# Optimization experiments

Measured on AMD Instinct MI355X. Metric: run time of the kernel, lower is better.

Reference implementation:

```python
import jax, jax.numpy as jnp
import numpy as np

N_TOKEN = 267735
CUTS = [0, 20000, 40000, 200000, 267735]
DIV = 4
D_MODEL = 1024
N_HEAD = 16
D_HEAD = 64
D_INNER = 4096
N_LAYER = 4
QLEN = 512
MLEN = 512
BSZ = 4
EPS = 1e-5


def _ln(x, g, b):
    mu = jnp.mean(x, axis=-1, keepdims=True)
    var = jnp.var(x, axis=-1, keepdims=True)
    return (x - mu) * jax.lax.rsqrt(var + EPS) * g + b


def _rel_shift(x):
    # x: [qlen, klen, bsz, n_head]
    q, k, b, n = x.shape
    x = jnp.pad(x, ((0, 0), (1, 0), (0, 0), (0, 0)))
    x = x.reshape(k + 1, q, b, n)[1:]
    return x.reshape(q, k, b, n)


def setup_inputs() -> dict:
    key = jax.random.key(0)
    ks = list(jax.random.split(key, 32))
    p = lambda i, shape: 0.02 * jax.random.normal(ks[i], shape, dtype=jnp.float32)
    inp = {}
    inp['input_ids'] = jax.random.randint(ks[0], (BSZ, QLEN), 0, N_TOKEN, dtype=jnp.int32)
    inp['mems'] = 0.05 * jax.random.normal(ks[1], (N_LAYER, MLEN, BSZ, D_MODEL), dtype=jnp.float32)
    # adaptive embedding: cluster tables + projections (div_val=4)
    for i in range(4):
        l, r = CUTS[i], CUTS[i + 1]
        d_i = D_MODEL // (DIV ** i)
        inp[f'emb{i}'] = p(2 + i, (r - l, d_i))
        inp[f'proj{i}'] = p(6 + i, (d_i, D_MODEL))
    H = N_HEAD * D_HEAD
    inp['qkv_W'] = p(10, (N_LAYER, D_MODEL, 3 * H))
    inp['r_W'] = p(11, (N_LAYER, D_MODEL, H))
    inp['o_W'] = p(12, (N_LAYER, H, D_MODEL))
    inp['r_w_bias'] = p(13, (N_LAYER, N_HEAD, D_HEAD))
    inp['r_r_bias'] = p(14, (N_LAYER, N_HEAD, D_HEAD))
    inp['ln1_g'] = jnp.ones((N_LAYER, D_MODEL), jnp.float32)
    inp['ln1_b'] = jnp.zeros((N_LAYER, D_MODEL), jnp.float32)
    inp['ff_w1'] = p(15, (N_LAYER, D_MODEL, D_INNER))
    inp['ff_b1'] = jnp.zeros((N_LAYER, D_INNER), jnp.float32)
    inp['ff_w2'] = p(16, (N_LAYER, D_INNER, D_MODEL))
    inp['ff_b2'] = jnp.zeros((N_LAYER, D_MODEL), jnp.float32)
    inp['ln2_g'] = jnp.ones((N_LAYER, D_MODEL), jnp.float32)
    inp['ln2_b'] = jnp.zeros((N_LAYER, D_MODEL), jnp.float32)
    return inp


def _forward(input_ids, mems, embs, projs, qkv_W, r_W, o_W, r_w_bias, r_r_bias,
             ln1_g, ln1_b, ff_w1, ff_b1, ff_w2, ff_b2, ln2_g, ln2_b):
    ids = input_ids.T  # [qlen, bsz]
    qlen, bsz = ids.shape
    mems = jax.lax.stop_gradient(mems)  # mems are detached in the original
    mlen = mems.shape[1]
    klen = qlen + mlen

    # --- adaptive embedding (masked gather + scatter-add, same math as boolean_mask/scatter_nd) ---
    flat = ids.reshape(-1)
    emb = jnp.zeros((flat.shape[0], D_MODEL), jnp.float32)
    for i in range(4):
        l, r = CUTS[i], CUTS[i + 1]
        mask = (flat >= l) & (flat < r)
        idx = jnp.clip(flat - l, 0, r - l - 1)
        e_i = jnp.einsum('id,de->ie', embs[i][idx], projs[i])
        emb = emb + jnp.where(mask[:, None], e_i, 0.0)
    word_emb = (emb * (D_MODEL ** 0.5)).reshape(qlen, bsz, D_MODEL)

    # --- sinusoidal relative positions, pos_seq = klen-1 .. 0 ---
    pos_seq = jnp.arange(klen - 1, -1, -1, dtype=jnp.float32)
    inv_freq = 1.0 / (10000.0 ** (jnp.arange(0, D_MODEL, 2, dtype=jnp.float32) / D_MODEL))
    sinusoid = jnp.einsum('i,j->ij', pos_seq, inv_freq)
    pos_emb = jnp.concatenate([jnp.sin(sinusoid), jnp.cos(sinusoid)], axis=-1)  # [klen, d_model]

    # causal mask over memory-extended keys: [qlen, klen]
    attn_mask = jnp.triu(jnp.ones((qlen, klen), jnp.float32), k=1 + mlen)
    mask4 = attn_mask[:, :, None, None]
    scale = 1.0 / (D_HEAD ** 0.5)

    h = word_emb
    for l in range(N_LAYER):
        cat = jnp.concatenate([mems[l], h], axis=0)  # [klen, bsz, d_model]
        w_heads = jnp.einsum('kbd,dh->kbh', cat, qkv_W[l])
        r_head_k = jnp.einsum('kd,dh->kh', pos_emb, r_W[l]).reshape(klen, N_HEAD, D_HEAD)
        q_h, k_h, v_h = jnp.split(w_heads, 3, axis=-1)
        q_h = q_h[-qlen:].reshape(qlen, bsz, N_HEAD, D_HEAD)
        k_h = k_h.reshape(klen, bsz, N_HEAD, D_HEAD)
        v_h = v_h.reshape(klen, bsz, N_HEAD, D_HEAD)
        AC = jnp.einsum('ibnd,jbnd->ijbn', q_h + r_w_bias[l], k_h)
        BD = _rel_shift(jnp.einsum('ibnd,jnd->ijbn', q_h + r_r_bias[l], r_head_k))
        score = (AC + BD) * scale
        score = score * (1.0 - mask4) - 1e30 * mask4
        prob = jax.nn.softmax(score, axis=1)
        attn_vec = jnp.einsum('ijbn,jbnd->ibnd', prob, v_h).reshape(qlen, bsz, N_HEAD * D_HEAD)
        attn_out = jnp.einsum('ibh,hd->ibd', attn_vec, o_W[l])
        h = _ln(h + attn_out, ln1_g[l], ln1_b[l])
        ff = jnp.einsum('ibf,fd->ibd', jax.nn.relu(jnp.einsum('ibd,df->ibf', h, ff_w1[l]) + ff_b1[l]), ff_w2[l]) + ff_b2[l]
        h = _ln(h + ff, ln2_g[l], ln2_b[l])

    return h.transpose(1, 0, 2)  # [bsz, qlen, d_model]


def reference(input_ids, mems, emb0, emb1, emb2, emb3, proj0, proj1, proj2, proj3,
              qkv_W, r_W, o_W, r_w_bias, r_r_bias, ln1_g, ln1_b,
              ff_w1, ff_b1, ff_w2, ff_b2, ln2_g, ln2_b):
    return _forward(input_ids, mems, (emb0, emb1, emb2, emb3), (proj0, proj1, proj2, proj3),
                    qkv_W, r_W, o_W, r_w_bias, r_r_bias, ln1_g, ln1_b,
                    ff_w1, ff_b1, ff_w2, ff_b2, ln2_g, ln2_b)
```

## Files before the change

kernel.cpp:

```cpp
#include <hip/hip_runtime.h>

typedef __attribute__((ext_vector_type(8))) short bf16x8;
typedef __attribute__((ext_vector_type(4))) float f32x4;

#define N_LAYER 4
#define QLEN 512
#define MLEN 512
#define KLEN 1024
#define BSZ 4
#define DM 1024
#define NH 16
#define DH 64
#define DINNER 4096
#define EK 1408
#define BDLD 1152

__device__ __forceinline__ unsigned short f2bf(float x) {
    unsigned u = __float_as_uint(x);
    u += 0x7fffu + ((u >> 16) & 1u);
    return (unsigned short)(u >> 16);
}
__device__ __forceinline__ float bf2f(unsigned short v) {
    return __uint_as_float(((unsigned)v) << 16);
}

__device__ __forceinline__ void gload16(const unsigned short* g, unsigned short* l) {
    __builtin_amdgcn_global_load_lds(
        (const __attribute__((address_space(1))) unsigned int*)g,
        (__attribute__((address_space(3))) unsigned int*)l, 16, 0, 0);
}

__device__ __forceinline__ bf16x8 lds_read8_sw(const unsigned short* base, int row, int cb) {
    return *(const bf16x8*)((const char*)base + row * 128 + (cb ^ ((row & 7) << 4)));
}

__global__ __launch_bounds__(256)
void transpose_all(const float* __restrict__ qkvWl, const float* __restrict__ rWl,
                   const float* __restrict__ oWl, const float* __restrict__ w1l,
                   const float* __restrict__ w2l,
                   unsigned short* __restrict__ qkvT, unsigned short* __restrict__ rT,
                   unsigned short* __restrict__ oT, unsigned short* __restrict__ w1T,
                   unsigned short* __restrict__ w2T) {
    __shared__ float tile[32][33];
    int id = blockIdx.x;
    const float* W; unsigned short* D; int K, N, bx, by;
    if (id < 3072)      { W = qkvWl; D = qkvT; K = 1024; N = 3072; bx = id % 96;  by = id / 96; }
    else if (id < 4096) { id -= 3072; W = rWl;  D = rT;  K = 1024; N = 1024; bx = id & 31; by = id >> 5; }
    else if (id < 5120) { id -= 4096; W = oWl;  D = oT;  K = 1024; N = 1024; bx = id & 31; by = id >> 5; }
    else if (id < 9216) { id -= 5120; W = w1l;  D = w1T; K = 1024; N = 4096; bx = id & 127; by = id >> 7; }
    else                { id -= 9216; W = w2l;  D = w2T; K = 4096; N = 1024; bx = id & 31; by = id >> 5; }
    const int tx = threadIdx.x & 31, ty = threadIdx.x >> 5;
#pragma unroll
    for (int i = 0; i < 4; ++i)
        tile[ty + i * 8][tx] = W[(size_t)(by * 32 + ty + i * 8) * N + bx * 32 + tx];
    __syncthreads();
#pragma unroll
    for (int i = 0; i < 4; ++i)
        D[(size_t)(bx * 32 + ty + i * 8) * K + by * 32 + tx] = f2bf(tile[tx][ty + i * 8]);
}

__global__ __launch_bounds__(256)
void transpose_pad(const float* __restrict__ W, unsigned short* __restrict__ dst,
                   int K, int N, int dstLD, int dstOff) {
    __shared__ float tile[32][33];
    const int tx = threadIdx.x & 31, ty = threadIdx.x >> 5;
    const int bx = blockIdx.x, by = blockIdx.y;
#pragma unroll
    for (int i = 0; i < 4; ++i) {
        int k = by * 32 + ty + i * 8;
        tile[ty + i * 8][tx] = (k < K) ? W[(size_t)k * N + bx * 32 + tx] : 0.f;
    }
    __syncthreads();
#pragma unroll
    for (int i = 0; i < 4; ++i) {
        int n = bx * 32 + ty + i * 8;
        int k = by * 32 + tx;
        dst[(size_t)n * dstLD + dstOff + k] = f2bf(tile[tx][ty + i * 8]);
    }
}

__global__ __launch_bounds__(256)
void emb_gather(const int* __restrict__ ids,
                const float* __restrict__ e0, const float* __restrict__ e1,
                const float* __restrict__ e2, const float* __restrict__ e3,
                unsigned short* __restrict__ embA) {
    const int chunk = blockIdx.x * 256 + threadIdx.x;
    if (chunk >= 2048 * 176) return;
    const int t = chunk / 176;
    const int e8 = (chunk - t * 176) * 8;
    const int i = t >> 2, b = t & 3;
    const int id = ids[b * QLEN + i];
    const float* src = nullptr;
    if (e8 < 1024) {
        if (id < 20000) src = e0 + (size_t)id * 1024 + e8;
    } else if (e8 < 1280) {
        if (id >= 20000 && id < 40000) src = e1 + (size_t)(id - 20000) * 256 + (e8 - 1024);
    } else if (e8 < 1344) {
        if (id >= 40000 && id < 200000) src = e2 + (size_t)(id - 40000) * 64 + (e8 - 1280);
    } else if (e8 < 1360) {
        if (id >= 200000) src = e3 + (size_t)(id - 200000) * 16 + (e8 - 1344);
    }
    uint4 o = {0u, 0u, 0u, 0u};
    if (src) {
        float4 v0 = *(const float4*)src;
        float4 v1 = *(const float4*)(src + 4);
        o.x = (unsigned)f2bf(v0.x * 32.f) | ((unsigned)f2bf(v0.y * 32.f) << 16);
        o.y = (unsigned)f2bf(v0.z * 32.f) | ((unsigned)f2bf(v0.w * 32.f) << 16);
        o.z = (unsigned)f2bf(v1.x * 32.f) | ((unsigned)f2bf(v1.y * 32.f) << 16);
        o.w = (unsigned)f2bf(v1.z * 32.f) | ((unsigned)f2bf(v1.w * 32.f) << 16);
    }
    *(uint4*)(embA + (size_t)t * EK + e8) = o;
}

template <int MODE, int BN>
__global__ __launch_bounds__(256)
void gemm_bt(const unsigned short* __restrict__ A, const unsigned short* __restrict__ BT,
             float* __restrict__ C, unsigned short* __restrict__ Cbf,
             const float* __restrict__ bias,
             const float* __restrict__ rwb, const float* __restrict__ rrb,
             unsigned short* __restrict__ Qw, unsigned short* __restrict__ Qr,
             unsigned short* __restrict__ Kb, unsigned short* __restrict__ VTb,
             int M, int N, int K) {
    constexpr int NF = BN / 32;
    __shared__ unsigned short lA[2][128 * 64];
    __shared__ unsigned short lB[2][BN * 64];
    const int tid = threadIdx.x;
    const int w = tid >> 6, l = tid & 63;
    const int lane15 = l & 15, lh = l >> 4;
    const int nwg = gridDim.x;
    const int cpx = nwg >> 3;
    const int swz = (blockIdx.x & 7) * cpx + (blockIdx.x >> 3);
    const int nbn = N / BN;
    const int bm = swz / nbn, bn = swz % nbn;
    const int wr = (w >> 1) * 64, wc = (w & 1) * (BN / 2);

    f32x4 acc[4][NF] = {};

    const unsigned short* gA = A + (size_t)(bm * 128) * K;
    const unsigned short* gB = BT + (size_t)(bn * BN) * K;

    auto stage = [&](int buf, int k0) {
#pragma unroll
        for (int s = 0; s < 4; ++s) {
            int g = tid + s * 256, row = g >> 3;
            gload16(gA + (size_t)row * K + k0 + ((g & 7) ^ (row & 7)) * 8,
                    lA[buf] + g * 8);
        }
#pragma unroll
        for (int s = 0; s < BN / 32; ++s) {
            int g = tid + s * 256, row = g >> 3;
            gload16(gB + (size_t)row * K + k0 + ((g & 7) ^ (row & 7)) * 8,
                    lB[buf] + g * 8);
        }
    };

    stage(0, 0);
    __syncthreads();
    int cur = 0;
    for (int k0 = 0; k0 < K; k0 += 64) {
        if (k0 + 64 < K) stage(cur ^ 1, k0 + 64);
        const unsigned short* cA = lA[cur];
        const unsigned short* cB = lB[cur];
#pragma unroll
        for (int kk = 0; kk < 2; ++kk) {
            bf16x8 af[4], bfr[NF];
#pragma unroll
            for (int f = 0; f < 4; ++f)
                af[f] = lds_read8_sw(cA, wr + f * 16 + lane15, kk * 64 + lh * 16);
#pragma unroll
            for (int f = 0; f < NF; ++f)
                bfr[f] = lds_read8_sw(cB, wc + f * 16 + lane15, kk * 64 + lh * 16);
#pragma unroll
            for (int mi = 0; mi < 4; ++mi)
#pragma unroll
                for (int ni = 0; ni < NF; ++ni)
                    acc[mi][ni] = __builtin_amdgcn_mfma_f32_16x16x32_bf16(
                        af[mi], bfr[ni], acc[mi][ni], 0, 0, 0);
        }
        __syncthreads();
        cur ^= 1;
    }

#pragma unroll
    for (int mi = 0; mi < 4; ++mi) {
        int rowb = bm * 128 + wr + mi * 16 + lh * 4;
#pragma unroll
        for (int ni = 0; ni < NF; ++ni) {
            int col = bn * BN + wc + ni * 16 + lane15;
#pragma unroll
            for (int r = 0; r < 4; ++r) {
                float x = acc[mi][ni][r];
                if (MODE == 0) {
                    C[(size_t)(rowb + r) * N + col] = x;
                } else if (MODE == 1) {
                    x += bias[col];
                    Cbf[(size_t)(rowb + r) * N + col] = f2bf(x > 0.f ? x : 0.f);
                } else if (MODE == 2) {
                    C[(size_t)(rowb + r) * N + col] = x + bias[col];
                } else if (MODE == 3) {
                    int j = rowb >> 2;
                    int bb_ = r;
                    if (col < 1024) {
                        if (j >= MLEN) {
                            int i = j - MLEN, n = col >> 6, d = col & 63;
                            size_t o = ((size_t)(bb_ * NH + n) * QLEN + i) * DH + d;
                            Qw[o] = f2bf(x + rwb[col]);
                            Qr[o] = f2bf(x + rrb[col]);
                        }
                    } else if (col < 2048) {
                        int c2 = col - 1024, n = c2 >> 6, d = c2 & 63;
                        Kb[((size_t)(bb_ * NH + n) * KLEN + j) * DH + d] = f2bf(x);
                    } else {
                        int c2 = col - 2048, n = c2 >> 6, d = c2 & 63;
                        VTb[((size_t)(bb_ * NH + n) * DH + d) * KLEN + j] = f2bf(x);
                    }
                } else {
                    int j = rowb + r;
                    int n = col >> 6, d = col & 63;
                    Kb[((size_t)n * KLEN + j) * DH + d] = f2bf(x);
                }
            }
        }
    }
}

__global__ __launch_bounds__(256)
void bd_gemm(const unsigned short* __restrict__ Qr, const unsigned short* __restrict__ Rb,
             unsigned short* __restrict__ BDs) {
    __shared__ unsigned short lA[128 * 64];
    __shared__ unsigned short lB[128 * 64];
    const int tid = threadIdx.x;
    const int w = tid >> 6, l = tid & 63;
    const int lane15 = l & 15, lh = l >> 4;
    const int blk = blockIdx.x;
    const int bn = blk & 63;
    const int tile = blk >> 6;
    const int mi_ = tile & 3, nj = tile >> 2;
    const int n = bn & 15;
    const int wr = (w >> 1) * 64, wc = (w & 1) * 64;

    const unsigned short* gA = Qr + (size_t)bn * QLEN * DH + (size_t)(mi_ * 128) * 64;
    const unsigned short* gB = Rb + (size_t)n * KLEN * DH + (size_t)(nj * 128) * 64;
#pragma unroll
    for (int s = 0; s < 4; ++s) {
        int g = tid + s * 256, row = g >> 3;
        gload16(gA + (size_t)row * 64 + ((g & 7) ^ (row & 7)) * 8, lA + g * 8);
        gload16(gB + (size_t)row * 64 + ((g & 7) ^ (row & 7)) * 8, lB + g * 8);
    }
    __syncthreads();
    f32x4 acc[4][4] = {};
#pragma unroll
    for (int kk = 0; kk < 2; ++kk) {
        bf16x8 af[4], bfr[4];
#pragma unroll
        for (int f = 0; f < 4; ++f) {
            af[f]  = lds_read8_sw(lA, wr + f * 16 + lane15, kk * 64 + lh * 16);
            bfr[f] = lds_read8_sw(lB, wc + f * 16 + lane15, kk * 64 + lh * 16);
        }
#pragma unroll
        for (int mi = 0; mi < 4; ++mi)
#pragma unroll
            for (int ni = 0; ni < 4; ++ni)
                acc[mi][ni] = __builtin_amdgcn_mfma_f32_16x16x32_bf16(
                    af[mi], bfr[ni], acc[mi][ni], 0, 0, 0);
    }
    unsigned short* out = BDs + (size_t)bn * 512 * BDLD;
#pragma unroll
    for (int mi = 0; mi < 4; ++mi) {
        int rowb = mi_ * 128 + wr + mi * 16 + lh * 4;
#pragma unroll
        for (int ni = 0; ni < 4; ++ni) {
            int col = nj * 128 + wc + ni * 16 + lane15;
#pragma unroll
            for (int r = 0; r < 4; ++r)
                out[(size_t)(rowb + r) * BDLD + col] = f2bf(acc[mi][ni][r]);
        }
    }
}

__global__ __launch_bounds__(256)
void pos_kernel(unsigned short* __restrict__ posbf) {
    const int p = blockIdx.x, tid = threadIdx.x;
    const float ps = (float)(KLEN - 1 - p);
    const float c = -2.0f * 9.210340371976184f / 1024.0f;
#pragma unroll
    for (int j4 = 0; j4 < 4; ++j4) {
        int j = tid + j4 * 256;
        int m = (j < 512) ? j : j - 512;
        float freq = __expf((float)m * c);
        float ang = ps * freq;
        float v = (j < 512) ? sinf(ang) : cosf(ang);
        posbf[(size_t)p * DM + j] = f2bf(v);
    }
}

__global__ __launch_bounds__(256)
void cat_kernel(const float* __restrict__ mem_l, const float* __restrict__ h,
                unsigned short* __restrict__ catbf) {
    const int t = blockIdx.x, tid = threadIdx.x;
    const float* src = (t < 2048) ? (mem_l + (size_t)t * DM) : (h + (size_t)(t - 2048) * DM);
    float4 v = ((const float4*)src)[tid];
    uint2 o;
    o.x = (unsigned)f2bf(v.x) | ((unsigned)f2bf(v.y) << 16);
    o.y = (unsigned)f2bf(v.z) | ((unsigned)f2bf(v.w) << 16);
    ((uint2*)(catbf + (size_t)t * DM))[tid] = o;
}

__global__ __launch_bounds__(64)
void attn_part(const unsigned short* __restrict__ Qw, const unsigned short* __restrict__ Qr,
               const unsigned short* __restrict__ Kb, const unsigned short* __restrict__ VTb,
               const unsigned short* __restrict__ BDs,
               unsigned short* __restrict__ Opart, float* __restrict__ ms) {
    __shared__ unsigned short lP[16 * 64];

    const int l = threadIdx.x;
    const int lane15 = l & 15, lh = l >> 4;
    const int blk = blockIdx.x;
    const int bn = blk & 63;
    const int rest = blk >> 6;
    const int rg = rest & 3;
    const int c = rest >> 2;

    const int offt[8] = {0, 3, 7, 11, 15, 20, 25, 30};
    const int nctt[8] = {3, 4, 4, 4, 5, 5, 5, 6};
    int it = 0;
#pragma unroll
    for (int i = 1; i < 8; ++i) if (c >= offt[i]) it = i;
    const int cl = c - offt[it];
    const int nck = nctt[it];
    const int ntiles = it + 9;
    const int jt0 = (cl * ntiles) / nck;
    const int jt1 = ((cl + 1) * ntiles) / nck;
    const int i0 = it * 64;
    const int rowl = rg * 16 + lh * 4;

    bf16x8 qw[2];
    {
        size_t qb = ((size_t)bn * QLEN + i0 + rg * 16 + lane15) * DH + lh * 8;
        qw[0] = *(const bf16x8*)(Qw + qb);
        qw[1] = *(const bf16x8*)(Qw + qb + 32);
    }

    const unsigned short* kp = Kb + (size_t)bn * KLEN * DH + (size_t)(jt0 * 64 + lane15) * DH + lh * 8;
    const unsigned short* vp = VTb + (size_t)bn * DH * KLEN + (size_t)lane15 * KLEN + jt0 * 64 + lh * 8;
    const unsigned short* bdp[4];
#pragma unroll
    for (int r = 0; r < 4; ++r) {
        int row = i0 + rowl + r;
        bdp[r] = BDs + (size_t)bn * 512 * BDLD + (size_t)row * BDLD
                 + (511 - row) + jt0 * 64 + lane15;
    }

    f32x4 oacc[4] = {};
    float mrow[4], srow[4];
#pragma unroll
    for (int r = 0; r < 4; ++r) { mrow[r] = -1e30f; srow[r] = 0.f; }

    for (int jt = jt0; jt < jt1; ++jt) {
        float bdv[4][4];
#pragma unroll
        for (int f = 0; f < 4; ++f)
#pragma unroll
            for (int r = 0; r < 4; ++r)
                bdv[f][r] = bf2f(bdp[r][16 * f]);

        bf16x8 kf[2][4];
#pragma unroll
        for (int f = 0; f < 4; ++f) {
            const unsigned short* p = kp + (size_t)(f * 16) * DH;
            kf[0][f] = *(const bf16x8*)p;
            kf[1][f] = *(const bf16x8*)(p + 32);
        }

        f32x4 sac[4] = {};
        __builtin_amdgcn_s_setprio(1);
#pragma unroll
        for (int kk = 0; kk < 2; ++kk)
#pragma unroll
            for (int f = 0; f < 4; ++f)
                sac[f] = __builtin_amdgcn_mfma_f32_16x16x32_bf16(qw[kk], kf[kk][f], sac[f], 0, 0, 0);
        __builtin_amdgcn_s_setprio(0);

        float pv[4][4];
        float tmax[4] = {-1e30f, -1e30f, -1e30f, -1e30f};
        const bool lastTile = (jt == it + 8);
#pragma unroll
        for (int f = 0; f < 4; ++f) {
            int lj = lane15 + 16 * f;
#pragma unroll
            for (int r = 0; r < 4; ++r) {
                float s = (sac[f][r] + bdv[f][r]) * 0.125f;
                if (lastTile && (lj > rowl + r)) s = -1e30f;
                pv[f][r] = s;
                tmax[r] = fmaxf(tmax[r], s);
            }
        }
#pragma unroll
        for (int off = 1; off < 16; off <<= 1)
#pragma unroll
            for (int r = 0; r < 4; ++r)
                tmax[r] = fmaxf(tmax[r], __shfl_xor(tmax[r], off));

        bf16x8 vf[2][4];
#pragma unroll
        for (int kk = 0; kk < 2; ++kk)
#pragma unroll
            for (int f = 0; f < 4; ++f)
                vf[kk][f] = *(const bf16x8*)(vp + (size_t)(f * 16) * KLEN + kk * 32);

        bool grow = false;
#pragma unroll
        for (int r = 0; r < 4; ++r) grow = grow || (tmax[r] > mrow[r] + 8.f);
        if (__any(grow)) {
#pragma unroll
            for (int r = 0; r < 4; ++r) {
                float nm = fmaxf(mrow[r], tmax[r]);
                float sc = __expf(mrow[r] - nm);
                mrow[r] = nm;
                srow[r] *= sc;
#pragma unroll
                for (int f = 0; f < 4; ++f) oacc[f][r] *= sc;
            }
        }
        float tsum[4];
#pragma unroll
        for (int r = 0; r < 4; ++r) {
            float ts = 0.f;
#pragma unroll
            for (int f = 0; f < 4; ++f) {
                float e = __expf(pv[f][r] - mrow[r]);
                pv[f][r] = e;
                ts += e;
            }
            tsum[r] = ts;
        }
#pragma unroll
        for (int off = 1; off < 16; off <<= 1)
#pragma unroll
            for (int r = 0; r < 4; ++r)
                tsum[r] += __shfl_xor(tsum[r], off);
#pragma unroll
        for (int r = 0; r < 4; ++r) srow[r] += tsum[r];

#pragma unroll
        for (int f = 0; f < 4; ++f)
#pragma unroll
            for (int r = 0; r < 4; ++r) {
                int row = lh * 4 + r, cb2 = (lane15 + 16 * f) * 2;
                *(unsigned short*)((char*)lP + row * 128 + (cb2 ^ ((row & 7) << 4))) =
                    f2bf(pv[f][r]);
            }
        bf16x8 pa[2];
        pa[0] = lds_read8_sw(lP, lane15, lh * 16);
        pa[1] = lds_read8_sw(lP, lane15, 64 + lh * 16);

        __builtin_amdgcn_s_setprio(1);
#pragma unroll
        for (int kk = 0; kk < 2; ++kk)
#pragma unroll
            for (int f = 0; f < 4; ++f)
                oacc[f] = __builtin_amdgcn_mfma_f32_16x16x32_bf16(pa[kk], vf[kk][f], oacc[f], 0, 0, 0);
        __builtin_amdgcn_s_setprio(0);

        kp += 64 * DH;
        vp += 64;
#pragma unroll
        for (int r = 0; r < 4; ++r) bdp[r] += 64;
    }

    const int slot = (bn * 8 + it) * 6 + cl;
    unsigned short* Op = Opart + (size_t)slot * 4096;
#pragma unroll
    for (int f = 0; f < 4; ++f)
#pragma unroll
        for (int r = 0; r < 4; ++r)
            Op[(rowl + r) * 64 + lane15 + 16 * f] = f2bf(oacc[f][r]);
    if (lane15 == 0) {
        float* msp = ms + (size_t)slot * 128;
#pragma unroll
        for (int r = 0; r < 4; ++r) {
            msp[rowl + r] = mrow[r];
            msp[64 + rowl + r] = srow[r];
        }
    }
}

__global__ __launch_bounds__(256)
void attn_merge(const unsigned short* __restrict__ Opart, const float* __restrict__ ms,
                unsigned short* __restrict__ avec) {
    const int blk = blockIdx.x;
    const int bn = blk & 63, it = blk >> 6;
    const int n = bn & 15, b = bn >> 4;
    const int nctt[8] = {3, 4, 4, 4, 5, 5, 5, 6};
    const int k = nctt[it];
    const int tid = threadIdx.x;
    const int r = tid >> 2, cq = (tid & 3) * 16;
    const int base_slot = (bn * 8 + it) * 6;

    float a[6], s[6];
    float M = -1e30f;
    for (int c = 0; c < 6; ++c) {
        if (c < k) {
            a[c] = ms[(size_t)(base_slot + c) * 128 + r];
            s[c] = ms[(size_t)(base_slot + c) * 128 + 64 + r];
            M = fmaxf(M, a[c]);
        } else { a[c] = -1e30f; s[c] = 0.f; }
    }
    float S = 0.f;
    for (int c = 0; c < 6; ++c) {
        a[c] = (c < k) ? __expf(a[c] - M) : 0.f;
        S += s[c] * a[c];
    }
    float acc[16];
#pragma unroll
    for (int j = 0; j < 16; ++j) acc[j] = 0.f;
    for (int c = 0; c < k; ++c) {
        const bf16x8* op = (const bf16x8*)(Opart + (size_t)(base_slot + c) * 4096 + r * 64 + cq);
        bf16x8 v0 = op[0], v1 = op[1];
        float ac = a[c];
#pragma unroll
        for (int j = 0; j < 8; ++j) {
            acc[j]     += ac * bf2f((unsigned short)v0[j]);
            acc[8 + j] += ac * bf2f((unsigned short)v1[j]);
        }
    }
    float inv = 1.0f / S;
    int t = (it * 64 + r) * 4 + b;
    unsigned short* dst = avec + (size_t)t * DM + n * 64 + cq;
#pragma unroll
    for (int j = 0; j < 16; ++j) dst[j] = f2bf(acc[j] * inv);
}

__global__ __launch_bounds__(256)
void ln_kernel(const float* __restrict__ hin, const float* __restrict__ res,
               const float* __restrict__ g, const float* __restrict__ bb,
               float* __restrict__ hout, unsigned short* __restrict__ hbf) {
    __shared__ float ls[8];
    const int t = blockIdx.x, tid = threadIdx.x;
    float4 x = ((const float4*)(hin + (size_t)t * DM))[tid];
    float4 rr = ((const float4*)(res + (size_t)t * DM))[tid];
    float v0 = x.x + rr.x, v1 = x.y + rr.y, v2 = x.z + rr.z, v3 = x.w + rr.w;
    float s = v0 + v1 + v2 + v3;
    float sq = v0 * v0 + v1 * v1 + v2 * v2 + v3 * v3;
#pragma unroll
    for (int off = 1; off < 64; off <<= 1) {
        s += __shfl_xor(s, off);
        sq += __shfl_xor(sq, off);
    }
    const int w = tid >> 6;
    if ((tid & 63) == 0) { ls[w] = s; ls[4 + w] = sq; }
    __syncthreads();
    s = ls[0] + ls[1] + ls[2] + ls[3];
    sq = ls[4] + ls[5] + ls[6] + ls[7];
    float mu = s * (1.f / 1024.f);
    float var = sq * (1.f / 1024.f) - mu * mu;
    float rstd = rsqrtf(var + 1e-5f);
    float y[4] = {v0, v1, v2, v3};
    float4 of;
    uint2 ob;
    float* op = &of.x;
#pragma unroll
    for (int j = 0; j < 4; ++j) {
        int d = tid * 4 + j;
        op[j] = (y[j] - mu) * rstd * g[d] + bb[d];
    }
    ob.x = (unsigned)f2bf(of.x) | ((unsigned)f2bf(of.y) << 16);
    ob.y = (unsigned)f2bf(of.z) | ((unsigned)f2bf(of.w) << 16);
    ((float4*)(hout + (size_t)t * DM))[tid] = of;
    ((uint2*)(hbf + (size_t)t * DM))[tid] = ob;
}

__global__ __launch_bounds__(256)
void out_kernel(const float* __restrict__ h, float* __restrict__ out) {
    const int t = blockIdx.x, tid = threadIdx.x;
    const int i = t >> 2, b = t & 3;
    ((float4*)(out + ((size_t)b * QLEN + i) * DM))[tid] =
        ((const float4*)(h + (size_t)t * DM))[tid];
}

extern "C" void kernel_launch(void* const* d_in, const int* in_sizes, int n_in,
                              void* d_out, int out_size, void* d_ws, size_t ws_size,
                              hipStream_t stream) {
    const int* ids = (const int*)d_in[0];
    const float* mems = (const float*)d_in[1];
    const float* embp[4] = {nullptr, nullptr, nullptr, nullptr};
    const float* projp[4] = {nullptr, nullptr, nullptr, nullptr};
    const long long esz[4] = {20000LL * 1024, 20000LL * 256, 160000LL * 64, 67735LL * 16};
    const long long psz[4] = {1024LL * 1024, 256LL * 1024, 64LL * 1024, 16LL * 1024};
    for (int idx = 2; idx <= 9 && idx < n_in; ++idx) {
        long long s = in_sizes[idx];
        for (int c = 0; c < 4; ++c) {
            if (s == esz[c]) embp[c] = (const float*)d_in[idx];
            else if (s == psz[c]) projp[c] = (const float*)d_in[idx];
        }
    }
    const float* qkvW = (const float*)d_in[10];
    const float* rW   = (const float*)d_in[11];
    const float* oW   = (const float*)d_in[12];
    const float* rwb  = (const float*)d_in[13];
    const float* rrb  = (const float*)d_in[14];
    const float* ln1g = (const float*)d_in[15];
    const float* ln1b = (const float*)d_in[16];
    const float* ffw1 = (const float*)d_in[17];
    const float* ffb1 = (const float*)d_in[18];
    const float* ffw2 = (const float*)d_in[19];
    const float* ffb2 = (const float*)d_in[20];
    const float* ln2g = (const float*)d_in[21];
    const float* ln2b = (const float*)d_in[22];

    size_t off = 0;
    char* base = (char*)d_ws;
    auto alloc = [&](size_t bytes) -> char* {
        char* p = base + off;
        off = (off + bytes + 255) & ~(size_t)255;
        return p;
    };
    unsigned short* qkvT  = (unsigned short*)alloc(3072ull * 1024 * 2);
    unsigned short* rT    = (unsigned short*)alloc(1024ull * 1024 * 2);
    unsigned short* oT    = (unsigned short*)alloc(1024ull * 1024 * 2);
    unsigned short* w1T   = (unsigned short*)alloc(4096ull * 1024 * 2);
    unsigned short* w2T   = (unsigned short*)alloc(1024ull * 4096 * 2);
    unsigned short* embA  = (unsigned short*)alloc(2048ull * EK * 2);
    unsigned short* embBT = (unsigned short*)alloc(1024ull * EK * 2);
    float* h              = (float*)alloc(2048ull * 1024 * 4);
    unsigned short* hbf   = (unsigned short*)alloc(2048ull * 1024 * 2);
    unsigned short* catb  = (unsigned short*)alloc(4096ull * 1024 * 2);
    unsigned short* posb  = (unsigned short*)alloc(1024ull * 1024 * 2);
    unsigned short* Qw    = (unsigned short*)alloc(4ull * 16 * 512 * 64 * 2);
    unsigned short* Qr    = (unsigned short*)alloc(4ull * 16 * 512 * 64 * 2);
    unsigned short* Kb    = (unsigned short*)alloc(4ull * 16 * 1024 * 64 * 2);
    unsigned short* VTb   = (unsigned short*)alloc(4ull * 16 * 1024 * 64 * 2);
    unsigned short* Rb    = (unsigned short*)alloc(16ull * 1024 * 64 * 2);
    unsigned short* avec  = (unsigned short*)alloc(2048ull * 1024 * 2);
    float* resid          = (float*)alloc(2048ull * 1024 * 4);
    unsigned short* ff1b  = (unsigned short*)alloc(2048ull * 4096 * 2);
    unsigned short* Opart = (unsigned short*)alloc(3072ull * 4096 * 2);
    float* msbuf          = (float*)alloc(3072ull * 128 * 4);
    unsigned short* BDs   = (unsigned short*)alloc(64ull * 512 * BDLD * 2);
    (void)ws_size; (void)out_size;

    emb_gather<<<(2048 * 176 + 255) / 256, 256, 0, stream>>>(
        ids, embp[0], embp[1], embp[2], embp[3], embA);
    transpose_pad<<<dim3(32, 32), 256, 0, stream>>>(projp[0], embBT, 1024, 1024, EK, 0);
    transpose_pad<<<dim3(32, 8),  256, 0, stream>>>(projp[1], embBT, 256,  1024, EK, 1024);
    transpose_pad<<<dim3(32, 2),  256, 0, stream>>>(projp[2], embBT, 64,   1024, EK, 1280);
    transpose_pad<<<dim3(32, 2),  256, 0, stream>>>(projp[3], embBT, 16,   1024, EK, 1344);
    pos_kernel<<<1024, 256, 0, stream>>>(posb);
    gemm_bt<0, 128><<<(2048 / 128) * (1024 / 128), 256, 0, stream>>>(
        embA, embBT, h, nullptr, nullptr, nullptr, nullptr, nullptr, nullptr, nullptr, nullptr,
        2048, 1024, EK);

    for (int l = 0; l < N_LAYER; ++l) {
        const float* qkvWl = qkvW + (size_t)l * 1024 * 3072;
        const float* rWl   = rW + (size_t)l * 1024 * 1024;
        const float* oWl   = oW + (size_t)l * 1024 * 1024;
        const float* w1l   = ffw1 + (size_t)l * 1024 * 4096;
        const float* w2l   = ffw2 + (size_t)l * 4096 * 1024;

        transpose_all<<<13312, 256, 0, stream>>>(qkvWl, rWl, oWl, w1l, w2l,
                                                 qkvT, rT, oT, w1T, w2T);

        cat_kernel<<<4096, 256, 0, stream>>>(mems + (size_t)l * 2048 * 1024, h, catb);

        gemm_bt<3, 128><<<(4096 / 128) * (3072 / 128), 256, 0, stream>>>(
            catb, qkvT, nullptr, nullptr, nullptr,
            rwb + l * 1024, rrb + l * 1024, Qw, Qr, Kb, VTb, 4096, 3072, 1024);

        gemm_bt<4, 64><<<(1024 / 128) * (1024 / 64), 256, 0, stream>>>(
            posb, rT, nullptr, nullptr, nullptr,
            nullptr, nullptr, nullptr, nullptr, Rb, nullptr, 1024, 1024, 1024);

        bd_gemm<<<64 * 32, 256, 0, stream>>>(Qr, Rb, BDs);

        attn_part<<<64 * 144, 64, 0, stream>>>(Qw, Qr, Kb, VTb, BDs, Opart, msbuf);
        attn_merge<<<512, 256, 0, stream>>>(Opart, msbuf, avec);

        gemm_bt<0, 64><<<(2048 / 128) * (1024 / 64), 256, 0, stream>>>(
            avec, oT, resid, nullptr, nullptr, nullptr, nullptr, nullptr, nullptr, nullptr, nullptr,
            2048, 1024, 1024);
        ln_kernel<<<2048, 256, 0, stream>>>(h, resid, ln1g + l * 1024, ln1b + l * 1024, h, hbf);

        gemm_bt<1, 128><<<(2048 / 128) * (4096 / 128), 256, 0, stream>>>(
            hbf, w1T, nullptr, ff1b, ffb1 + l * 4096, nullptr, nullptr, nullptr, nullptr, nullptr, nullptr,
            2048, 4096, 1024);
        gemm_bt<2, 64><<<(2048 / 128) * (1024 / 64), 256, 0, stream>>>(
            ff1b, w2T, resid, nullptr, ffb2 + l * 1024, nullptr, nullptr, nullptr, nullptr, nullptr, nullptr,
            2048, 1024, 4096);
        ln_kernel<<<2048, 256, 0, stream>>>(h, resid, ln2g + l * 1024, ln2b + l * 1024, h, hbf);
    }

    out_kernel<<<2048, 256, 0, stream>>>(h, (float*)d_out);
}
```

Measured before the change: 1.141 ms.

## Widen weight transpose tiles to 64x64 and single-buffer GEMM LDS staging

The weight transpose kernel moves from 32x32 to 64x64 tiles, reading with float4 loads and writing eight packed bf16 values per 16-byte store. This cuts the block count and makes the global traffic wider. Separately, the GEMM drops LDS double buffering and instead loads each K tile and then synchronises before computing. That halves LDS use, which may allow more resident blocks, but load latency is no longer overlapped with MFMA work inside a block.

Result: slower. 1.183 ms (+3.7%).

```diff
diff --git a/kernel.cpp b/kernel.cpp
--- a/kernel.cpp
+++ b/kernel.cpp
@@ -41,22 +41,33 @@
                    unsigned short* __restrict__ qkvT, unsigned short* __restrict__ rT,
                    unsigned short* __restrict__ oT, unsigned short* __restrict__ w1T,
                    unsigned short* __restrict__ w2T) {
-    __shared__ float tile[32][33];
+    __shared__ float tile[64][65];
     int id = blockIdx.x;
     const float* W; unsigned short* D; int K, N, bx, by;
-    if (id < 3072)      { W = qkvWl; D = qkvT; K = 1024; N = 3072; bx = id % 96;  by = id / 96; }
-    else if (id < 4096) { id -= 3072; W = rWl;  D = rT;  K = 1024; N = 1024; bx = id & 31; by = id >> 5; }
-    else if (id < 5120) { id -= 4096; W = oWl;  D = oT;  K = 1024; N = 1024; bx = id & 31; by = id >> 5; }
-    else if (id < 9216) { id -= 5120; W = w1l;  D = w1T; K = 1024; N = 4096; bx = id & 127; by = id >> 7; }
-    else                { id -= 9216; W = w2l;  D = w2T; K = 4096; N = 1024; bx = id & 31; by = id >> 5; }
-    const int tx = threadIdx.x & 31, ty = threadIdx.x >> 5;
-#pragma unroll
-    for (int i = 0; i < 4; ++i)
-        tile[ty + i * 8][tx] = W[(size_t)(by * 32 + ty + i * 8) * N + bx * 32 + tx];
+    if (id < 768)       { W = qkvWl; D = qkvT; K = 1024; N = 3072; bx = id % 48; by = id / 48; }
+    else if (id < 1024) { id -= 768;  W = rWl;  D = rT;  K = 1024; N = 1024; bx = id & 15; by = id >> 4; }
+    else if (id < 1280) { id -= 1024; W = oWl;  D = oT;  K = 1024; N = 1024; bx = id & 15; by = id >> 4; }
+    else if (id < 2304) { id -= 1280; W = w1l;  D = w1T; K = 1024; N = 4096; bx = id & 63; by = id >> 6; }
+    else                { id -= 2304; W = w2l;  D = w2T; K = 4096; N = 1024; bx = id & 15; by = id >> 4; }
+    const int tid = threadIdx.x;
+#pragma unroll
+    for (int s = 0; s < 4; ++s) {
+        int idx = s * 256 + tid;
+        int kr = idx >> 4, c4 = (idx & 15) * 4;
+        float4 v = *(const float4*)(W + (size_t)(by * 64 + kr) * N + bx * 64 + c4);
+        tile[kr][c4] = v.x; tile[kr][c4 + 1] = v.y;
+        tile[kr][c4 + 2] = v.z; tile[kr][c4 + 3] = v.w;
+    }
     __syncthreads();
 #pragma unroll
-    for (int i = 0; i < 4; ++i)
-        D[(size_t)(bx * 32 + ty + i * 8) * K + by * 32 + tx] = f2bf(tile[tx][ty + i * 8]);
+    for (int s = 0; s < 2; ++s) {
+        int idx = s * 256 + tid;
+        int nl = idx >> 3, k8 = (idx & 7) * 8;
+        unsigned short tmp[8];
+#pragma unroll
+        for (int j = 0; j < 8; ++j) tmp[j] = f2bf(tile[k8 + j][nl]);
+        *(uint4*)(D + (size_t)(bx * 64 + nl) * K + by * 64 + k8) = *(uint4*)tmp;
+    }
 }
 
 __global__ __launch_bounds__(256)
@@ -122,8 +133,8 @@
              unsigned short* __restrict__ Kb, unsigned short* __restrict__ VTb,
              int M, int N, int K) {
     constexpr int NF = BN / 32;
-    __shared__ unsigned short lA[2][128 * 64];
-    __shared__ unsigned short lB[2][BN * 64];
+    __shared__ unsigned short lA[128 * 64];
+    __shared__ unsigned short lB[BN * 64];
     const int tid = threadIdx.x;
     const int w = tid >> 6, l = tid & 63;
     const int lane15 = l & 15, lh = l >> 4;
@@ -139,37 +150,30 @@
     const unsigned short* gA = A + (size_t)(bm * 128) * K;
     const unsigned short* gB = BT + (size_t)(bn * BN) * K;
 
-    auto stage = [&](int buf, int k0) {
+    for (int k0 = 0; k0 < K; k0 += 64) {
+        __syncthreads();
 #pragma unroll
         for (int s = 0; s < 4; ++s) {
             int g = tid + s * 256, row = g >> 3;
             gload16(gA + (size_t)row * K + k0 + ((g & 7) ^ (row & 7)) * 8,
-                    lA[buf] + g * 8);
+                    lA + g * 8);
         }
 #pragma unroll
         for (int s = 0; s < BN / 32; ++s) {
             int g = tid + s * 256, row = g >> 3;
             gload16(gB + (size_t)row * K + k0 + ((g & 7) ^ (row & 7)) * 8,
-                    lB[buf] + g * 8);
-        }
-    };
-
-    stage(0, 0);
-    __syncthreads();
-    int cur = 0;
-    for (int k0 = 0; k0 < K; k0 += 64) {
-        if (k0 + 64 < K) stage(cur ^ 1, k0 + 64);
-        const unsigned short* cA = lA[cur];
-        const unsigned short* cB = lB[cur];
+                    lB + g * 8);
+        }
+        __syncthreads();
 #pragma unroll
         for (int kk = 0; kk < 2; ++kk) {
             bf16x8 af[4], bfr[NF];
 #pragma unroll
             for (int f = 0; f < 4; ++f)
-                af[f] = lds_read8_sw(cA, wr + f * 16 + lane15, kk * 64 + lh * 16);
+                af[f] = lds_read8_sw(lA, wr + f * 16 + lane15, kk * 64 + lh * 16);
 #pragma unroll
             for (int f = 0; f < NF; ++f)
-                bfr[f] = lds_read8_sw(cB, wc + f * 16 + lane15, kk * 64 + lh * 16);
+                bfr[f] = lds_read8_sw(lB, wc + f * 16 + lane15, kk * 64 + lh * 16);
 #pragma unroll
             for (int mi = 0; mi < 4; ++mi)
 #pragma unroll
@@ -177,8 +181,6 @@
                     acc[mi][ni] = __builtin_amdgcn_mfma_f32_16x16x32_bf16(
                         af[mi], bfr[ni], acc[mi][ni], 0, 0, 0);
         }
-        __syncthreads();
-        cur ^= 1;
     }
 
 #pragma unroll
@@ -657,8 +659,8 @@
         const float* w1l   = ffw1 + (size_t)l * 1024 * 4096;
         const float* w2l   = ffw2 + (size_t)l * 4096 * 1024;
 
-        transpose_all<<<13312, 256, 0, stream>>>(qkvWl, rWl, oWl, w1l, w2l,
-                                                 qkvT, rT, oT, w1T, w2T);
+        transpose_all<<<3328, 256, 0, stream>>>(qkvWl, rWl, oWl, w1l, w2l,
+                                                qkvT, rT, oT, w1T, w2T);
 
         cat_kernel<<<4096, 256, 0, stream>>>(mems + (size_t)l * 2048 * 1024, h, catb);
 
```
